# Kernel optimization log

Measured on AMD Instinct MI355X. Metric: run time of the kernel, lower is better.

Reference implementation:

```python
import jax, jax.numpy as jnp
import numpy as np

NEIGHBOR_RATE = 0.1  # neighbor_rate init arg
LEAKY_SLOPE = 0.2
NEG_INF = -1.0e9


def setup_inputs() -> dict:
    key = jax.random.key(0)
    k1, k2, k3, k4 = jax.random.split(key, 4)
    B, N, Din, H, hd = 4, 2048, 128, 4, 32  # output_dim = H*hd = 128
    h = jax.random.normal(k1, (B, N, Din), jnp.float32)
    adj = jax.random.uniform(k2, (B, N, N), jnp.float32)
    # stacked per-head params: W[k] in [Din, hd], a[k] in [2*hd]
    w_bound = 1.0 / np.sqrt(Din)
    a_bound = 1.0 / np.sqrt(2 * hd)
    W = jax.random.uniform(k3, (H, Din, hd), jnp.float32, -w_bound, w_bound)
    a = jax.random.uniform(k4, (H, 2 * hd), jnp.float32, -a_bound, a_bound)
    return {"h": h, "adj": adj, "W": W, "a": a}


def reference(h, adj, W, a):
    B, N, _ = h.shape
    H, _, hd = W.shape
    k = int(NEIGHBOR_RATE * N)  # num_neighbors
    # Wh: [B,H,N,hd]
    Wh = jnp.einsum('bnf,hfd->bhnd', h, W)
    # cat([Wh_i, Wh_j]) @ a  ==  Wh_i @ a[:hd] + Wh_j @ a[hd:] (broadcast trick)
    s_i = jnp.einsum('bhnd,hd->bhn', Wh, a[:, :hd])
    s_j = jnp.einsum('bhnd,hd->bhn', Wh, a[:, hd:])
    e = jax.nn.leaky_relu(s_i[..., :, None] + s_j[..., None, :], LEAKY_SLOPE)  # [B,H,N,N]
    # top-k mask along last (neighbor) axis, built by scatter like torch .scatter_
    _, idx = jax.lax.top_k(e, k)  # [B,H,N,k]
    row_mask = lambda i: jnp.zeros((N,), jnp.bool_).at[i].set(True)
    mask = jax.vmap(row_mask)(idx.reshape(-1, k)).reshape(e.shape)
    masked = jnp.where(mask, e, NEG_INF)
    attn = jax.nn.softmax(masked, axis=-1) * adj[:, None]  # [B,H,N,N]
    hp = jnp.einsum('bhnm,bhmd->bhnd', attn, Wh)
    # concat heads on feature dim -> [B,N,H*hd]
    return hp.transpose(0, 2, 1, 3).reshape(B, N, H * hd)
```

## Files before the change

### kernel.cpp

```cpp
#include <hip/hip_runtime.h>
#include <hip/hip_bf16.h>
#include <cmath>

#define BB 4
#define NN 2048
#define DIN 128
#define HH 4
#define HD 32
#define KSEL 204
#define BH (BB*HH)
#define KPAD 256
#define CRPB 4

typedef __attribute__((ext_vector_type(8))) short short8;
typedef __attribute__((ext_vector_type(4))) short short4v;
typedef __attribute__((ext_vector_type(4))) float float4v;

static __device__ inline short f2bf(float x) {
    __hip_bfloat16 b = __float2bfloat16(x);
    return __builtin_bit_cast(short, b);
}

__global__ __launch_bounds__(256) void hs_kernel(const float* __restrict__ h,
                                                 const float* __restrict__ W,
                                                 const float* __restrict__ a,
                                                 short* __restrict__ hbf,
                                                 float* __restrict__ si, float* __restrict__ sj) {
    int g = blockIdx.x;
    int bh = g >> 3, chunk = g & 7;
    int b = bh >> 2, hh = bh & 3;
    int t = threadIdx.x;
    {
        const float4* src = (const float4*)h + (size_t)g * 2048;
        short4v* dst = (short4v*)hbf + (size_t)g * 2048;
#pragma unroll
        for (int q = 0; q < 8; ++q) {
            float4 x = src[q * 256 + t];
            short4v r;
            r[0] = f2bf(x.x); r[1] = f2bf(x.y); r[2] = f2bf(x.z); r[3] = f2bf(x.w);
            dst[q * 256 + t] = r;
        }
    }
    __shared__ float w1[128], w2[128];
    {
        int f = t & 127, half = t >> 7;
        const float* Wp = W + (size_t)hh * (DIN * HD) + f * HD;
        const float* ap = a + hh * 64 + half * 32;
        float acc = 0.f;
#pragma unroll
        for (int d = 0; d < 32; ++d) acc += Wp[d] * ap[d];
        if (half == 0) w1[f] = acc; else w2[f] = acc;
    }
    __syncthreads();
    int n = chunk * 256 + t;
    const float4* hr = (const float4*)(h + ((size_t)b * NN + n) * DIN);
    float s1 = 0.f, s2 = 0.f;
#pragma unroll 8
    for (int q = 0; q < 32; ++q) {
        float4 x = hr[q];
        s1 += x.x * w1[q*4] + x.y * w1[q*4+1] + x.z * w1[q*4+2] + x.w * w1[q*4+3];
        s2 += x.x * w2[q*4] + x.y * w2[q*4+1] + x.z * w2[q*4+2] + x.w * w2[q*4+3];
    }
    int o = bh * NN + n;
    si[o] = s1; sj[o] = s2;
}

__global__ __launch_bounds__(256) void wh_kernel(const short* __restrict__ hbf,
                                                 const float* __restrict__ W,
                                                 short* __restrict__ Whg) {
    int bh = blockIdx.x >> 4, rtile = blockIdx.x & 15;
    int b = bh >> 2, hh = bh & 3;
    __shared__ short WT[32][136];
    int t = threadIdx.x;
    for (int e = t; e < 32 * 128; e += 256) {
        int n = e >> 7, k = e & 127;
        WT[n][k] = f2bf(W[(size_t)hh * (DIN * HD) + k * HD + n]);
    }
    __syncthreads();
    int w = t >> 6, lane = t & 63, mr = lane & 15, quad = lane >> 4;
    int row_base = rtile * 128;
#pragma unroll
    for (int q = 0; q < 4; ++q) {
        int tt = w * 4 + q;
        int rt = tt >> 1, ct = tt & 1;
        int row0 = row_base + rt * 16;
        const short* hrow = hbf + ((size_t)b * NN + row0 + mr) * DIN + quad * 8;
        float4v acc = {0.f, 0.f, 0.f, 0.f};
#pragma unroll
        for (int ks = 0; ks < 4; ++ks) {
            short8 afr = *(const short8*)(hrow + ks * 32);
            short8 bfr = *(const short8*)&WT[ct * 16 + mr][ks * 32 + quad * 8];
            acc = __builtin_amdgcn_mfma_f32_16x16x32_bf16(afr, bfr, acc, 0, 0, 0);
        }
#pragma unroll
        for (int r = 0; r < 4; ++r) {
            int rowg = row0 + quad * 4 + r;
            Whg[((size_t)bh * NN + rowg) * HD + ct * 16 + mr] = f2bf(acc[r]);
        }
    }
}

__global__ __launch_bounds__(1024) void select_kernel(
        const float* __restrict__ sj, const short* __restrict__ Whg,
        int* __restrict__ idxsel, float* __restrict__ sjsel,
        float* __restrict__ sjmax, short* __restrict__ Whsel) {
    int bh = blockIdx.x;
    int t = threadIdx.x, lane = t & 63, w = t >> 6;
    __shared__ float sv[NN];
    __shared__ int hist16[16][256];
    __shared__ int binInfo[2];
    __shared__ int wtot[4];
    __shared__ int wtotg[16], wtote[16], woffg[16], woffe[16];
    __shared__ float wmax[16];
    __shared__ int idxLDS[KSEL];

    const float* s = sj + (size_t)bh * NN;
    int j0 = t * 2;
    float x0 = s[j0], x1 = s[j0 + 1];
    sv[j0] = x0; sv[j0 + 1] = x1;
    unsigned u0 = __builtin_bit_cast(unsigned, x0);
    unsigned u1 = __builtin_bit_cast(unsigned, x1);
    u0 = (u0 & 0x80000000u) ? ~u0 : (u0 | 0x80000000u);
    u1 = (u1 & 0x80000000u) ? ~u1 : (u1 | 0x80000000u);
    float lmax = fmaxf(x0, x1);
#pragma unroll
    for (int off = 32; off >= 1; off >>= 1) lmax = fmaxf(lmax, __shfl_xor(lmax, off));
    if (lane == 0) wmax[w] = lmax;
    __syncthreads();
    if (t == 0) {
        float m = wmax[0];
#pragma unroll
        for (int i = 1; i < 16; ++i) m = fmaxf(m, wmax[i]);
        sjmax[bh] = m;
    }

    unsigned prefix = 0;
    int need = KSEL;
#pragma unroll
    for (int shift = 24; shift >= 0; shift -= 8) {
        ((int*)hist16)[t] = 0; ((int*)hist16)[t + 1024] = 0;
        ((int*)hist16)[t + 2048] = 0; ((int*)hist16)[t + 3072] = 0;
        __syncthreads();
        unsigned hmask = (shift < 24) ? (0xFFFFFFFFu << (shift + 8)) : 0u;
        if (((u0 ^ prefix) & hmask) == 0) atomicAdd(&hist16[w][(u0 >> shift) & 255], 1);
        if (((u1 ^ prefix) & hmask) == 0) atomicAdd(&hist16[w][(u1 >> shift) & 255], 1);
        __syncthreads();
        int sc = 0, hv = 0, bb = 0;
        if (t < 256) {
            bb = 255 - t;
            hv = 0;
#pragma unroll
            for (int i = 0; i < 16; ++i) hv += hist16[i][bb];
            sc = hv;
#pragma unroll
            for (int off = 1; off < 64; off <<= 1) {
                int u = __shfl_up(sc, off);
                if (lane >= off) sc += u;
            }
            if (lane == 63) wtot[w] = sc;
        }
        __syncthreads();
        if (t < 256) {
            int woffset = 0;
#pragma unroll
            for (int i = 0; i < 4; ++i) woffset += (i < w) ? wtot[i] : 0;
            int incl = sc + woffset;
            int excl = incl - hv;
            if (incl >= need && excl < need) {
                binInfo[0] = bb;
                binInfo[1] = excl;
            }
        }
        __syncthreads();
        prefix |= ((unsigned)binInfo[0]) << shift;
        need -= binInfo[1];
        __syncthreads();
    }
    unsigned T = prefix;
    int n_gt = KSEL - need;

    int cg = (u0 > T ? 1 : 0) + (u1 > T ? 1 : 0);
    int ce = (u0 == T ? 1 : 0) + (u1 == T ? 1 : 0);
    int sg = cg, se = ce;
#pragma unroll
    for (int off = 1; off < 64; off <<= 1) {
        int ug = __shfl_up(sg, off), ue = __shfl_up(se, off);
        if (lane >= off) { sg += ug; se += ue; }
    }
    if (lane == 63) { wtotg[w] = sg; wtote[w] = se; }
    __syncthreads();
    if (t == 0) {
        int rg = 0, re = 0;
#pragma unroll
        for (int i = 0; i < 16; ++i) {
            woffg[i] = rg; rg += wtotg[i];
            woffe[i] = re; re += wtote[i];
        }
    }
    __syncthreads();
    int pg = woffg[w] + sg - cg;
    int te = woffe[w] + se - ce;
    {
        unsigned kk[2] = {u0, u1};
#pragma unroll
        for (int r = 0; r < 2; ++r) {
            int j = j0 + r;
            if (kk[r] > T) {
                idxsel[bh * KSEL + pg] = j;
                sjsel[bh * KSEL + pg] = sv[j];
                idxLDS[pg] = j;
                pg++;
            } else if (kk[r] == T) {
                if (te < need) {
                    int pos = n_gt + te;
                    idxsel[bh * KSEL + pos] = j;
                    sjsel[bh * KSEL + pos] = sv[j];
                    idxLDS[pos] = j;
                }
                te++;
            }
        }
    }
    __syncthreads();
    for (int e = t; e < HD * KPAD; e += 1024) {
        int d = e >> 8, jj = e & 255;
        short v = 0;
        if (jj < KSEL) v = Whg[((size_t)bh * NN + idxLDS[jj]) * HD + d];
        Whsel[((size_t)bh * HD + d) * KPAD + jj] = v;
    }
}

__global__ __launch_bounds__(256) void coef_kernel(
        const float* __restrict__ adj, const float* __restrict__ si,
        const int* __restrict__ idxsel, const float* __restrict__ sjsel,
        const float* __restrict__ sjmax, short* __restrict__ PS,
        float* __restrict__ invZ) {
    int b = blockIdx.x >> 9;
    int chunk = blockIdx.x & 511;
    __shared__ float adjbuf[CRPB][NN];
    __shared__ int   idxS[HH][KPAD];
    __shared__ float sjS[HH][KPAD];
    __shared__ float smaxS[HH];
    int t = threadIdx.x, w = t >> 6, lane = t & 63;
    int i0 = chunk * CRPB;
    const float* adjb = adj + (size_t)b * NN * NN;
    {
        const float4* src = (const float4*)(adjb + (size_t)i0 * NN);
        float4* dst = (float4*)adjbuf;
#pragma unroll
        for (int q = 0; q < CRPB * 2; ++q)
            dst[q * 256 + t] = src[q * 256 + t];
    }
    for (int e = t; e < HH * KPAD; e += 256) {
        int hh = e >> 8, jj = e & 255;
        bool v = jj < KSEL;
        idxS[hh][jj] = v ? idxsel[(b * HH + hh) * KSEL + jj] : 0;
        sjS[hh][jj]  = v ? sjsel[(b * HH + hh) * KSEL + jj] : -1e30f;
    }
    if (t < HH) smaxS[t] = sjmax[b * HH + t];
    __syncthreads();
    int bh = b * HH + w;
    float smax = smaxS[w];
#pragma unroll
    for (int r = 0; r < CRPB; ++r) {
        const float* ab = adjbuf[r];
        int i = i0 + r;
        float siv = si[(size_t)bh * NN + i];
        float m = siv + smax;
        m = (m >= 0.f) ? m : 0.2f * m;
        float z = 0.f;
        short* prow = PS + ((size_t)bh * NN + i) * KPAD;
#pragma unroll
        for (int k = 0; k < 2; ++k) {
            int jj = k * 128 + lane * 2;
            int ja = idxS[w][jj], jb = idxS[w][jj + 1];
            float ava = ab[ja], avb = ab[jb];
            float ea = siv + sjS[w][jj];
            float eb = siv + sjS[w][jj + 1];
            ea = (ea >= 0.f) ? ea : 0.2f * ea;
            eb = (eb >= 0.f) ? eb : 0.2f * eb;
            float ca = __expf(ea - m);
            float cb = __expf(eb - m);
            z += ca + cb;
            short2 p;
            p.x = f2bf(ca * ava);
            p.y = f2bf(cb * avb);
            *(short2*)&prow[jj] = p;
        }
#pragma unroll
        for (int off = 32; off >= 1; off >>= 1) z += __shfl_xor(z, off);
        if (lane == 0) invZ[(size_t)bh * NN + i] = 1.0f / z;
    }
}

__global__ __launch_bounds__(256) void pv_kernel(
        const short* __restrict__ PS, const short* __restrict__ Whsel,
        const float* __restrict__ invZ, float* __restrict__ out) {
    int bh = blockIdx.x >> 6, tile = blockIdx.x & 63;
    int b = bh >> 2, hh = bh & 3;
    int t = threadIdx.x, w = t >> 6, lane = t & 63;
    int mr = lane & 15, quad = lane >> 4;
    int mi = w >> 1, ni = w & 1;
    int i0 = tile * 32;
    const short* pA = PS + ((size_t)bh * NN + i0 + mi * 16 + mr) * KPAD + quad * 8;
    const short* pB = Whsel + ((size_t)bh * HD + ni * 16 + mr) * KPAD + quad * 8;
    float4v acc = {0.f, 0.f, 0.f, 0.f};
#pragma unroll
    for (int ks = 0; ks < 8; ++ks) {
        short8 afr = *(const short8*)(pA + ks * 32);
        short8 bfr = *(const short8*)(pB + ks * 32);
        acc = __builtin_amdgcn_mfma_f32_16x16x32_bf16(afr, bfr, acc, 0, 0, 0);
    }
#pragma unroll
    for (int r = 0; r < 4; ++r) {
        int i = i0 + mi * 16 + quad * 4 + r;
        int d = ni * 16 + mr;
        out[((size_t)(b * NN + i)) * (HH * HD) + hh * HD + d] =
            acc[r] * invZ[(size_t)bh * NN + i];
    }
}

extern "C" void kernel_launch(void* const* d_in, const int* in_sizes, int n_in,
                              void* d_out, int out_size, void* d_ws, size_t ws_size,
                              hipStream_t stream) {
    const float* h   = (const float*)d_in[0];
    const float* adj = (const float*)d_in[1];
    const float* W   = (const float*)d_in[2];
    const float* a   = (const float*)d_in[3];
    float* out = (float*)d_out;

    float* si     = (float*)d_ws;
    float* sj     = si + (size_t)BH * NN;
    float* invZ   = sj + (size_t)BH * NN;
    float* sjsel  = invZ + (size_t)BH * NN;
    float* sjmax  = sjsel + (size_t)BH * KSEL;
    int*   idxsel = (int*)(sjmax + 16);
    short* hbf    = (short*)(idxsel + (size_t)BH * KSEL);
    short* Whg    = hbf + (size_t)BB * NN * DIN;
    short* Whsel  = Whg + (size_t)BH * NN * HD;
    short* PS     = Whsel + (size_t)BH * HD * KPAD;

    hs_kernel<<<BH * 8, 256, 0, stream>>>(h, W, a, hbf, si, sj);
    wh_kernel<<<BH * 16, 256, 0, stream>>>(hbf, W, Whg);
    select_kernel<<<BH, 1024, 0, stream>>>(sj, Whg, idxsel, sjsel, sjmax, Whsel);
    coef_kernel<<<BB * (NN / CRPB), 256, 0, stream>>>(adj, si, idxsel, sjsel, sjmax, PS, invZ);
    pv_kernel<<<BH * 64, 256, 0, stream>>>(PS, Whsel, invZ, out);
}
```

Measured before the change: 141.3 us.

## Fuse coefficient and PV kernels, keeping attention tiles in LDS

Merges coef_kernel and pv_kernel into one attn2_kernel. Each block builds the bf16 masked attention coefficients for 16 rows × 4 heads in shared memory and feeds them straight to MFMA against Whsel fragments preloaded in registers. This removes the global PS and invZ round-trips and one kernel launch. In exchange there are far fewer blocks (512 instead of 2048), and each block streams its adj rows in four serialized chunks separated by barriers, which may reduce memory-level parallelism on the dominant adj read.

```diff
diff --git a/kernel.cpp b/kernel.cpp
--- a/kernel.cpp
+++ b/kernel.cpp
@@ -10,7 +10,7 @@
 #define KSEL 204
 #define BH (BB*HH)
 #define KPAD 256
-#define CRPB 4
+#define KST 264
 
 typedef __attribute__((ext_vector_type(8))) short short8;
 typedef __attribute__((ext_vector_type(4))) short short4v;
@@ -230,27 +230,22 @@
     }
 }
 
-__global__ __launch_bounds__(256) void coef_kernel(
+__global__ __launch_bounds__(256) void attn2_kernel(
         const float* __restrict__ adj, const float* __restrict__ si,
         const int* __restrict__ idxsel, const float* __restrict__ sjsel,
-        const float* __restrict__ sjmax, short* __restrict__ PS,
-        float* __restrict__ invZ) {
-    int b = blockIdx.x >> 9;
-    int chunk = blockIdx.x & 511;
-    __shared__ float adjbuf[CRPB][NN];
+        const float* __restrict__ sjmax, const short* __restrict__ Whsel,
+        float* __restrict__ out) {
+    int b = blockIdx.x >> 7;
+    int tile = blockIdx.x & 127;
+    __shared__ float adjbuf[4][NN];
+    __shared__ short PSb[HH][16][KST];
     __shared__ int   idxS[HH][KPAD];
     __shared__ float sjS[HH][KPAD];
+    __shared__ float invZS[HH][16];
     __shared__ float smaxS[HH];
     int t = threadIdx.x, w = t >> 6, lane = t & 63;
-    int i0 = chunk * CRPB;
-    const float* adjb = adj + (size_t)b * NN * NN;
-    {
-        const float4* src = (const float4*)(adjb + (size_t)i0 * NN);
-        float4* dst = (float4*)adjbuf;
-#pragma unroll
-        for (int q = 0; q < CRPB * 2; ++q)
-            dst[q * 256 + t] = src[q * 256 + t];
-    }
+    int mr = lane & 15, quad = lane >> 4;
+
     for (int e = t; e < HH * KPAD; e += 256) {
         int hh = e >> 8, jj = e & 255;
         bool v = jj < KSEL;
@@ -258,65 +253,86 @@
         sjS[hh][jj]  = v ? sjsel[(b * HH + hh) * KSEL + jj] : -1e30f;
     }
     if (t < HH) smaxS[t] = sjmax[b * HH + t];
-    __syncthreads();
+
+    short8 bfr[2][8];
+    {
+        const short* wp = Whsel + (size_t)((b * HH + w) * HD) * KPAD;
+#pragma unroll
+        for (int ni = 0; ni < 2; ++ni)
+#pragma unroll
+            for (int ks = 0; ks < 8; ++ks)
+                bfr[ni][ks] = *(const short8*)(wp + (size_t)(ni * 16 + mr) * KPAD + ks * 32 + quad * 8);
+    }
+
+    int i0 = tile * 16;
+    const float* adjb = adj + (size_t)b * NN * NN;
+    {
+        const float4* src = (const float4*)(adjb + (size_t)i0 * NN);
+        float4* dst = (float4*)adjbuf;
+#pragma unroll
+        for (int q = 0; q < 8; ++q)
+            dst[q * 256 + t] = src[q * 256 + t];
+    }
+    __syncthreads();
+
     int bh = b * HH + w;
     float smax = smaxS[w];
-#pragma unroll
-    for (int r = 0; r < CRPB; ++r) {
-        const float* ab = adjbuf[r];
-        int i = i0 + r;
-        float siv = si[(size_t)bh * NN + i];
-        float m = siv + smax;
-        m = (m >= 0.f) ? m : 0.2f * m;
-        float z = 0.f;
-        short* prow = PS + ((size_t)bh * NN + i) * KPAD;
-#pragma unroll
-        for (int k = 0; k < 2; ++k) {
-            int jj = k * 128 + lane * 2;
-            int ja = idxS[w][jj], jb = idxS[w][jj + 1];
-            float ava = ab[ja], avb = ab[jb];
-            float ea = siv + sjS[w][jj];
-            float eb = siv + sjS[w][jj + 1];
-            ea = (ea >= 0.f) ? ea : 0.2f * ea;
-            eb = (eb >= 0.f) ? eb : 0.2f * eb;
-            float ca = __expf(ea - m);
-            float cb = __expf(eb - m);
-            z += ca + cb;
-            short2 p;
-            p.x = f2bf(ca * ava);
-            p.y = f2bf(cb * avb);
-            *(short2*)&prow[jj] = p;
-        }
-#pragma unroll
-        for (int off = 32; off >= 1; off >>= 1) z += __shfl_xor(z, off);
-        if (lane == 0) invZ[(size_t)bh * NN + i] = 1.0f / z;
-    }
-}
-
-__global__ __launch_bounds__(256) void pv_kernel(
-        const short* __restrict__ PS, const short* __restrict__ Whsel,
-        const float* __restrict__ invZ, float* __restrict__ out) {
-    int bh = blockIdx.x >> 6, tile = blockIdx.x & 63;
-    int b = bh >> 2, hh = bh & 3;
-    int t = threadIdx.x, w = t >> 6, lane = t & 63;
-    int mr = lane & 15, quad = lane >> 4;
-    int mi = w >> 1, ni = w & 1;
-    int i0 = tile * 32;
-    const short* pA = PS + ((size_t)bh * NN + i0 + mi * 16 + mr) * KPAD + quad * 8;
-    const short* pB = Whsel + ((size_t)bh * HD + ni * 16 + mr) * KPAD + quad * 8;
-    float4v acc = {0.f, 0.f, 0.f, 0.f};
-#pragma unroll
-    for (int ks = 0; ks < 8; ++ks) {
-        short8 afr = *(const short8*)(pA + ks * 32);
-        short8 bfr = *(const short8*)(pB + ks * 32);
-        acc = __builtin_amdgcn_mfma_f32_16x16x32_bf16(afr, bfr, acc, 0, 0, 0);
-    }
-#pragma unroll
-    for (int r = 0; r < 4; ++r) {
-        int i = i0 + mi * 16 + quad * 4 + r;
-        int d = ni * 16 + mr;
-        out[((size_t)(b * NN + i)) * (HH * HD) + hh * HD + d] =
-            acc[r] * invZ[(size_t)bh * NN + i];
+    for (int s = 0; s < 4; ++s) {
+#pragma unroll
+        for (int r = 0; r < 4; ++r) {
+            int i_loc = s * 4 + r;
+            int i = i0 + i_loc;
+            float siv = si[(size_t)bh * NN + i];
+            float m = siv + smax;
+            m = (m >= 0.f) ? m : 0.2f * m;
+            float z = 0.f;
+            short* prow = &PSb[w][i_loc][0];
+#pragma unroll
+            for (int k = 0; k < 2; ++k) {
+                int jj = k * 128 + lane * 2;
+                int ja = idxS[w][jj], jb = idxS[w][jj + 1];
+                float ava = adjbuf[r][ja], avb = adjbuf[r][jb];
+                float ea = siv + sjS[w][jj];
+                float eb = siv + sjS[w][jj + 1];
+                ea = (ea >= 0.f) ? ea : 0.2f * ea;
+                eb = (eb >= 0.f) ? eb : 0.2f * eb;
+                float ca = __expf(ea - m);
+                float cb = __expf(eb - m);
+                z += ca + cb;
+                short2 p;
+                p.x = f2bf(ca * ava);
+                p.y = f2bf(cb * avb);
+                *(short2*)&prow[jj] = p;
+            }
+#pragma unroll
+            for (int off = 32; off >= 1; off >>= 1) z += __shfl_xor(z, off);
+            if (lane == 0) invZS[w][i_loc] = 1.0f / z;
+        }
+        if (s < 3) {
+            __syncthreads();
+            const float4* src = (const float4*)(adjb + (size_t)(i0 + (s + 1) * 4) * NN);
+            float4* dst = (float4*)adjbuf;
+#pragma unroll
+            for (int q = 0; q < 8; ++q)
+                dst[q * 256 + t] = src[q * 256 + t];
+            __syncthreads();
+        }
+    }
+#pragma unroll
+    for (int ni = 0; ni < 2; ++ni) {
+        float4v acc = {0.f, 0.f, 0.f, 0.f};
+#pragma unroll
+        for (int ks = 0; ks < 8; ++ks) {
+            short8 afr = *(const short8*)&PSb[w][mr][ks * 32 + quad * 8];
+            acc = __builtin_amdgcn_mfma_f32_16x16x32_bf16(afr, bfr[ni][ks], acc, 0, 0, 0);
+        }
+#pragma unroll
+        for (int r = 0; r < 4; ++r) {
+            int i_loc = quad * 4 + r;
+            int d = ni * 16 + mr;
+            out[((size_t)(b * NN + i0 + i_loc)) * (HH * HD) + w * HD + d] =
+                acc[r] * invZS[w][i_loc];
+        }
     }
 }
 
@@ -331,18 +347,15 @@
 
     float* si     = (float*)d_ws;
     float* sj     = si + (size_t)BH * NN;
-    float* invZ   = sj + (size_t)BH * NN;
-    float* sjsel  = invZ + (size_t)BH * NN;
+    float* sjsel  = sj + (size_t)BH * NN;
     float* sjmax  = sjsel + (size_t)BH * KSEL;
     int*   idxsel = (int*)(sjmax + 16);
     short* hbf    = (short*)(idxsel + (size_t)BH * KSEL);
     short* Whg    = hbf + (size_t)BB * NN * DIN;
     short* Whsel  = Whg + (size_t)BH * NN * HD;
-    short* PS     = Whsel + (size_t)BH * HD * KPAD;
 
     hs_kernel<<<BH * 8, 256, 0, stream>>>(h, W, a, hbf, si, sj);
     wh_kernel<<<BH * 16, 256, 0, stream>>>(hbf, W, Whg);
     select_kernel<<<BH, 1024, 0, stream>>>(sj, Whg, idxsel, sjsel, sjmax, Whsel);
-    coef_kernel<<<BB * (NN / CRPB), 256, 0, stream>>>(adj, si, idxsel, sjsel, sjmax, PS, invZ);
-    pv_kernel<<<BH * 64, 256, 0, stream>>>(PS, Whsel, invZ, out);
-}
+    attn2_kernel<<<BB * 128, 256, 0, stream>>>(adj, si, idxsel, sjsel, sjmax, Whsel, out);
+}
```

Result: faster. 133.4 us (-5.6%).
